# Kernel optimization log

Hardware: AMD Instinct MI355X
Metric: run time of the kernel (lower is better)

## Reference

```python
import jax, jax.numpy as jnp
import numpy as np
from jax import lax

DIM = 384
HEADS = 8

def setup_inputs() -> dict:
    key = jax.random.key(0)
    ks = jax.random.split(key, 7)
    B, C, H, W = 4, DIM, 128, 128
    x = jax.random.normal(ks[0], (B, C, H, W), dtype=jnp.float32)
    y = jax.random.normal(ks[1], (B, C, H, W), dtype=jnp.float32)
    s1 = 1.0 / np.sqrt(C)
    Wq = jax.random.normal(ks[2], (C, C), dtype=jnp.float32) * s1          # 1x1 conv [out,in]
    Wkv = jax.random.normal(ks[3], (2 * C, C), dtype=jnp.float32) * s1     # 1x1 conv
    Wdw = jax.random.normal(ks[4], (3 * C, 1, 3, 3), dtype=jnp.float32) * (1.0 / 3.0)  # depthwise 3x3
    Wproj = jax.random.normal(ks[5], (C, C), dtype=jnp.float32) * s1       # 1x1 conv
    temperature = jnp.ones((HEADS, 1, 1), dtype=jnp.float32)
    return {"x": x, "y": y, "Wq": Wq, "Wkv": Wkv, "Wdw": Wdw,
            "Wproj": Wproj, "temperature": temperature}


def _conv1x1(x, W):
    # x: [b,c,h,w], W: [o,c] -> [b,o,h,w]
    return jnp.einsum('bchw,oc->bohw', x, W)


def _l2norm(t, eps=1e-12):
    n = jnp.sqrt(jnp.sum(t * t, axis=-1, keepdims=True))
    return t / jnp.maximum(n, eps)


def reference(x, y, Wq, Wkv, Wdw, Wproj, temperature):
    b, c, h, w = x.shape
    q = _conv1x1(x, Wq)                     # [b,c,h,w]
    kv = _conv1x1(y, Wkv)                   # [b,2c,h,w]
    qkv = jnp.concatenate([q, kv], axis=1)  # [b,3c,h,w]
    qkv = lax.conv_general_dilated(
        qkv, Wdw, window_strides=(1, 1), padding='SAME',
        dimension_numbers=('NCHW', 'OIHW', 'NCHW'),
        feature_group_count=3 * c)
    q, k, v = jnp.split(qkv, 3, axis=1)
    cp = c // HEADS
    hw = h * w
    # b (head c) h w -> b head c (h w)
    q = q.reshape(b, HEADS, cp, hw)
    k = k.reshape(b, HEADS, cp, hw)
    v = v.reshape(b, HEADS, cp, hw)
    q = _l2norm(q)
    k = _l2norm(k)
    attn = jnp.einsum('bhcn,bhdn->bhcd', q, k) * temperature  # [b,head,cp,cp]
    attn = jax.nn.softmax(attn, axis=-1)
    out = jnp.einsum('bhcd,bhdn->bhcn', attn, v)              # [b,head,cp,hw]
    out = out.reshape(b, c, h, w)
    return _conv1x1(out, Wproj)
```

## Files before the change

### kernel.cpp

```cpp
#include <hip/hip_runtime.h>
#include <hip/hip_bf16.h>

#define DIM 384
#define HEADS 8
#define CP 48
#define NB 4
#define HIMG 128
#define WIMG 128
#define HW 16384

using bf16 = __hip_bfloat16;

typedef __attribute__((ext_vector_type(8))) short bf16x8;
typedef __attribute__((ext_vector_type(4))) float f32x4;

__device__ __forceinline__ float lo_bf(unsigned u){ union{unsigned i; float f;} c; c.i = u<<16; return c.f; }
__device__ __forceinline__ float hi_bf(unsigned u){ union{unsigned i; float f;} c; c.i = u & 0xffff0000u; return c.f; }
__device__ __forceinline__ bf16 f2bf(float v){ return __float2bfloat16(v); }
__device__ __forceinline__ unsigned short bfbits(float v){ union{ bf16 h; unsigned short u; } c; c.h = f2bf(v); return c.u; }

__device__ __forceinline__ float4 load4f(const float* p){ return *(const float4*)p; }
__device__ __forceinline__ float4 load4f(const bf16* p){
  uint2 u = *(const uint2*)p;
  float4 r; r.x = lo_bf(u.x); r.y = hi_bf(u.x); r.z = lo_bf(u.y); r.w = hi_bf(u.y); return r;
}

__device__ __forceinline__ void st(float* p, float v){ *p = v; }
__device__ __forceinline__ void st(bf16* p, float v){ *p = f2bf(v); }

#define GLD_LDS16(g, l) __builtin_amdgcn_global_load_lds( \
    (const __attribute__((address_space(1))) void*)(g), \
    (__attribute__((address_space(3))) void*)(l), 16, 0, 0)

__global__ __launch_bounds__(256) void convert_w(
    const float* __restrict__ Wq, const float* __restrict__ Wkv,
    bf16* __restrict__ Wq_bf, bf16* __restrict__ Wkv_bf)
{
  int idx = (blockIdx.x*256 + threadIdx.x) * 2;
  const int NQ = DIM*DIM;
  const int NKV = 2*DIM*DIM;
  if (idx < NQ) {
    unsigned u = (unsigned)bfbits(Wq[idx]) | ((unsigned)bfbits(Wq[idx+1]) << 16);
    *(unsigned*)(Wq_bf + idx) = u;
  } else {
    int j = idx - NQ;
    if (j < NKV) {
      unsigned u = (unsigned)bfbits(Wkv[j]) | ((unsigned)bfbits(Wkv[j+1]) << 16);
      *(unsigned*)(Wkv_bf + j) = u;
    }
  }
}

template<typename TIn>
__global__ __launch_bounds__(256) void transpose_cast(
    const TIn* __restrict__ in0, const TIn* __restrict__ in1,
    bf16* __restrict__ out0, bf16* __restrict__ out1,
    long inBatchStride, long outBatchStride)
{
  const int zb = blockIdx.z;
  const TIn* in = (zb < NB) ? in0 : in1;
  bf16* outp = (zb < NB) ? out0 : out1;
  const int b = zb & 3;
  const int n0 = blockIdx.x * 64;
  const int c0 = blockIdx.y * 64;
  const TIn* inb = in + (long)b * inBatchStride;
  bf16* outb = outp + (long)b * outBatchStride;

  __shared__ float tile[64][66];
  const int t = threadIdx.x;
#pragma unroll
  for (int i = 0; i < 4; ++i) {
    int g = i*256 + t;
    int r = g >> 4, c4 = g & 15;
    float4 v = load4f(inb + (long)(c0 + r)*HW + n0 + c4*4);
    tile[r][c4*4+0] = v.x; tile[r][c4*4+1] = v.y;
    tile[r][c4*4+2] = v.z; tile[r][c4*4+3] = v.w;
  }
  __syncthreads();
#pragma unroll
  for (int i = 0; i < 8; ++i) {
    int g = i*256 + t;
    int n = g >> 5, cu = g & 31;
    unsigned u = (unsigned)bfbits(tile[cu*2][n]) | ((unsigned)bfbits(tile[cu*2+1][n]) << 16);
    *(unsigned*)(outb + (long)(n0 + n)*DIM + c0 + cu*2) = u;
  }
}

template<typename TOut>
__global__ __launch_bounds__(256) void gemm_mfma(
    const bf16* __restrict__ A, long aStride,
    const bf16* __restrict__ Bt, TOut* __restrict__ C, int M, int K)
{
  const int b  = blockIdx.z;
  const int m0 = blockIdx.y * 128;
  const int n0 = blockIdx.x * 128;
  const bf16* Ab  = A  + (long)b * aStride;
  const bf16* Btb = Bt + (long)b * (long)HW * K;
  TOut* Cb = C + (long)b * (long)M * HW;

  __shared__ short As[128*64];
  __shared__ short Bs[128*64];

  const int t = threadIdx.x;
  const int w = t >> 6, lane = t & 63;
  const int quad = lane >> 4, l16 = lane & 15;
  const int wm = (w >> 1) * 64, wn = (w & 1) * 64;

  const bf16* gA[4]; const bf16* gB[4];
#pragma unroll
  for (int i = 0; i < 4; ++i) {
    int f = w*256 + i*64 + lane;
    int r = f >> 3, p = f & 7;
    int c = p ^ (r & 7);
    gA[i] = Ab  + (long)(m0 + r)*K + c*8;
    gB[i] = Btb + (long)(n0 + r)*K + c*8;
  }

  f32x4 acc[4][4] = {};

  for (int k0 = 0; k0 < K; k0 += 64) {
#pragma unroll
    for (int i = 0; i < 4; ++i) {
      GLD_LDS16(gA[i], As + (w*256 + i*64)*8);
      GLD_LDS16(gB[i], Bs + (w*256 + i*64)*8);
      gA[i] += 64; gB[i] += 64;
    }
    __syncthreads();
#pragma unroll
    for (int kk = 0; kk < 2; ++kk) {
      bf16x8 af[4], bfr[4];
      const int sw = (kk*4 + quad) ^ (l16 & 7);
#pragma unroll
      for (int mt = 0; mt < 4; ++mt) {
        af[mt]  = *(const bf16x8*)(As + (wm + mt*16 + l16)*64 + sw*8);
        bfr[mt] = *(const bf16x8*)(Bs + (wn + mt*16 + l16)*64 + sw*8);
      }
#pragma unroll
      for (int mt = 0; mt < 4; ++mt)
#pragma unroll
        for (int nt = 0; nt < 4; ++nt)
          acc[mt][nt] = __builtin_amdgcn_mfma_f32_16x16x32_bf16(af[mt], bfr[nt], acc[mt][nt], 0, 0, 0);
    }
    __syncthreads();
  }

#pragma unroll
  for (int mt = 0; mt < 4; ++mt)
#pragma unroll
    for (int nt = 0; nt < 4; ++nt)
#pragma unroll
      for (int j = 0; j < 4; ++j) {
        int row = m0 + wm + mt*16 + quad*4 + j;
        int col = n0 + wn + nt*16 + l16;
        st(Cb + (long)row*HW + col, acc[mt][nt][j]);
      }
}

__global__ __launch_bounds__(256) void dwconv_inplace(
    bf16* __restrict__ qb, bf16* __restrict__ kvb,
    const float* __restrict__ Wdw, float* __restrict__ ssq)
{
  const int ch = blockIdx.x;
  const int b  = blockIdx.y;
  bf16* plane = (ch < DIM) ? qb + ((long)b*DIM + ch)*HW
                           : kvb + ((long)b*2*DIM + (ch - DIM))*HW;
  float w9[9];
#pragma unroll
  for (int i = 0; i < 9; ++i) w9[i] = Wdw[ch*9 + i];

  __shared__ bf16 t_[128*140];
  const int t = threadIdx.x;
#pragma unroll
  for (int i = 0; i < 16; ++i) {
    int g = i*256 + t;
    int r = g >> 5, c4 = g & 31;
    *(uint2*)&t_[r*140 + c4*4] = *(const uint2*)(plane + r*128 + c4*4);
  }
  __syncthreads();

  const int r = t >> 1, half = t & 1, cbase = half*64;
  const float mtop = (r > 0)   ? 1.f : 0.f;
  const float mbot = (r < 127) ? 1.f : 0.f;
  const int rt = (r > 0)   ? r-1 : r;
  const int rb = (r < 127) ? r+1 : r;

  float a0,a1,a2,b0,b1,b2,c0,c1,c2;
#define LD3(cc, A, B, Cv) { A = __bfloat162float(t_[rt*140 + (cc)]) * mtop; \
                            B = __bfloat162float(t_[r*140 + (cc)]); \
                            Cv = __bfloat162float(t_[rb*140 + (cc)]) * mbot; }
  if (cbase == 0) { a0=b0=c0=0.f; } else LD3(cbase-1, a0, b0, c0);
  LD3(cbase,   a1, b1, c1);
  LD3(cbase+1, a2, b2, c2);

  float ss = 0.f;
  unsigned outu[32];
#pragma unroll 4
  for (int j = 0; j < 64; ++j) {
    float o = w9[0]*a0 + w9[1]*a1 + w9[2]*a2
            + w9[3]*b0 + w9[4]*b1 + w9[5]*b2
            + w9[6]*c0 + w9[7]*c1 + w9[8]*c2;
    ss += o*o;
    unsigned short ob = bfbits(o);
    if (j & 1) outu[j>>1] |= ((unsigned)ob << 16); else outu[j>>1] = ob;
    a0=a1; a1=a2; b0=b1; b1=b2; c0=c1; c1=c2;
    int nc = cbase + j + 2;
    if (nc <= 127) { LD3(nc, a2, b2, c2) } else { a2=b2=c2=0.f; }
  }
#undef LD3

#pragma unroll
  for (int i = 0; i < 8; ++i)
    *(uint4*)(plane + r*128 + cbase + i*8) = *(uint4*)&outu[i*4];

  if (ch < 2*DIM) {
#pragma unroll
    for (int off = 32; off; off >>= 1) ss += __shfl_down(ss, off);
    __shared__ float wsum[4];
    if ((t & 63) == 0) wsum[t >> 6] = ss;
    __syncthreads();
    if (t == 0) ssq[b*2*DIM + ch] = wsum[0]+wsum[1]+wsum[2]+wsum[3];
  }
}

__global__ __launch_bounds__(512) void s_mfma(
    const bf16* __restrict__ qd, const bf16* __restrict__ kd,
    float* __restrict__ Sp)
{
  const int split = blockIdx.x;
  const int h = blockIdx.y, b = blockIdx.z;
  const int t = threadIdx.x, w = t >> 6, lane = t & 63;
  const int quad = lane >> 4, l16 = lane & 15;
  const bf16* qp = qd + ((long)b*DIM + h*CP)*HW;
  const bf16* kp = kd + ((long)b*DIM + h*CP)*HW;
  const int nbase = (split*8 + w) * 256;

  f32x4 acc[3][3] = {};
  for (int ks = 0; ks < 8; ++ks) {
    const int n = nbase + ks*32 + quad*8;
    bf16x8 aq[3], bk[3];
#pragma unroll
    for (int i = 0; i < 3; ++i) {
      aq[i] = *(const bf16x8*)(qp + (long)(i*16 + l16)*HW + n);
      bk[i] = *(const bf16x8*)(kp + (long)(i*16 + l16)*HW + n);
    }
#pragma unroll
    for (int i = 0; i < 3; ++i)
#pragma unroll
      for (int j = 0; j < 3; ++j)
        acc[i][j] = __builtin_amdgcn_mfma_f32_16x16x32_bf16(aq[i], bk[j], acc[i][j], 0, 0, 0);
  }

  __shared__ float Sred[8][CP*CP];
#pragma unroll
  for (int i = 0; i < 3; ++i)
#pragma unroll
    for (int j = 0; j < 3; ++j)
#pragma unroll
      for (int rr = 0; rr < 4; ++rr)
        Sred[w][(i*16 + quad*4 + rr)*CP + j*16 + l16] = acc[i][j][rr];
  __syncthreads();

  float* out = Sp + (long)split*(NB*HEADS*CP*CP) + ((long)(b*HEADS + h))*CP*CP;
  for (int g = t; g < CP*CP; g += 512) {
    float s = 0.f;
#pragma unroll
    for (int ww = 0; ww < 8; ++ww) s += Sred[ww][g];
    out[g] = s;
  }
}

__global__ __launch_bounds__(64) void softmax_attn(
    float* __restrict__ Sp, const float* __restrict__ ssq,
    const float* __restrict__ temp)
{
  const int bhc = blockIdx.x;
  const int c = bhc % CP;
  const int h = (bhc / CP) % HEADS;
  const int b = bhc / (CP * HEADS);
  const int lane = threadIdx.x;
  const long rowoff = ((long)(b*HEADS + h))*CP*CP + c*CP;
  const float rq = rsqrtf(ssq[b*2*DIM + h*CP + c]);
  const float tmp = temp[h];
  float logit = -1e30f;
  if (lane < CP) {
    float s = 0.f;
#pragma unroll
    for (int sl = 0; sl < 8; ++sl) s += Sp[(long)sl*(NB*HEADS*CP*CP) + rowoff + lane];
    float rk = rsqrtf(ssq[b*2*DIM + DIM + h*CP + lane]);
    logit = s * rq * rk * tmp;
  }
  float m = logit;
#pragma unroll
  for (int off = 32; off; off >>= 1) m = fmaxf(m, __shfl_down(m, off));
  m = __shfl(m, 0);
  float e = (lane < CP) ? __expf(logit - m) : 0.f;
  float s = e;
#pragma unroll
  for (int off = 32; off; off >>= 1) s += __shfl_down(s, off);
  s = __shfl(s, 0);
  if (lane < CP) Sp[rowoff + lane] = e / s;
}

__global__ __launch_bounds__(256) void w2fold(
    const float* __restrict__ attn, const float* __restrict__ Wproj,
    bf16* __restrict__ W2)
{
  const int ot = blockIdx.x;
  const int h  = blockIdx.y;
  const int b  = blockIdx.z;
  __shared__ float at[CP][CP];
  __shared__ float wp[128][CP];
  const int t = threadIdx.x;
  const float* Ap = attn + ((long)(b*HEADS + h))*CP*CP;
#pragma unroll
  for (int i = 0; i < 9; ++i) {
    int idx = t + 256*i;
    at[idx / CP][idx % CP] = Ap[idx];
  }
#pragma unroll
  for (int i = 0; i < 24; ++i) {
    int idx = t + 256*i;
    int o = idx / CP, c = idx % CP;
    wp[o][c] = Wproj[(long)(ot*128 + o)*DIM + h*CP + c];
  }
  __syncthreads();
#pragma unroll
  for (int i = 0; i < 24; ++i) {
    int idx = t + 256*i;
    int o = idx / CP, d = idx % CP;
    float a = 0.f;
#pragma unroll
    for (int c = 0; c < CP; ++c) a += wp[o][c] * at[c][d];
    W2[((long)b*DIM + ot*128 + o)*DIM + h*CP + d] = f2bf(a);
  }
}

extern "C" void kernel_launch(void* const* d_in, const int* in_sizes, int n_in,
                              void* d_out, int out_size, void* d_ws, size_t ws_size,
                              hipStream_t stream) {
  const float* x     = (const float*)d_in[0];
  const float* y     = (const float*)d_in[1];
  const float* Wq    = (const float*)d_in[2];
  const float* Wkv   = (const float*)d_in[3];
  const float* Wdw   = (const float*)d_in[4];
  const float* Wproj = (const float*)d_in[5];
  const float* temp  = (const float*)d_in[6];
  float* out = (float*)d_out;

  char* ws = (char*)d_ws;
  const long SZ_T  = 50331648L;
  bf16* xT    = (bf16*)(ws + 0L);
  bf16* yT    = (bf16*)(ws + SZ_T);
  bf16* q_bf  = (bf16*)(ws + 2*SZ_T);
  bf16* kv_bf = (bf16*)(ws + 3*SZ_T);
  char* tail  = ws + 5*SZ_T;
  bf16* Wq_bf  = (bf16*)(tail);
  bf16* Wkv_bf = (bf16*)(tail + 294912L);
  float* Sp    = (float*)(tail);
  bf16* W2_bf  = (bf16*)(tail + 294912L);
  float* ssq   = (float*)(tail + 2359296L);
  bf16* vdT    = xT;
  bf16* vd     = kv_bf + (long)DIM*HW;

  convert_w<<<864, 256, 0, stream>>>(Wq, Wkv, Wq_bf, Wkv_bf);
  transpose_cast<float><<<dim3(HW/64, DIM/64, 8), 256, 0, stream>>>(
      x, y, xT, yT, (long)DIM*HW, (long)HW*DIM);
  gemm_mfma<bf16><<<dim3(HW/128, DIM/128, NB), 256, 0, stream>>>(
      Wq_bf, 0, xT, q_bf, DIM, DIM);
  gemm_mfma<bf16><<<dim3(HW/128, 2*DIM/128, NB), 256, 0, stream>>>(
      Wkv_bf, 0, yT, kv_bf, 2*DIM, DIM);
  dwconv_inplace<<<dim3(3*DIM, NB), 256, 0, stream>>>(q_bf, kv_bf, Wdw, ssq);
  transpose_cast<bf16><<<dim3(HW/64, DIM/64, NB), 256, 0, stream>>>(
      vd, nullptr, vdT, nullptr, (long)2*DIM*HW, (long)HW*DIM);
  s_mfma<<<dim3(8, HEADS, NB), 512, 0, stream>>>(q_bf, kv_bf, Sp);
  softmax_attn<<<dim3(NB*HEADS*CP), 64, 0, stream>>>(Sp, ssq, temp);
  w2fold<<<dim3(3, HEADS, NB), 256, 0, stream>>>(Sp, Wproj, W2_bf);
  gemm_mfma<float><<<dim3(HW/128, DIM/128, NB), 256, 0, stream>>>(
      W2_bf, (long)DIM*DIM, vdT, out, DIM, DIM);
}
```

Before: 560.7 us.

## Replace transpose+GEMM with panel GEMM that transposes B in LDS

```diff
diff --git a/kernel.cpp b/kernel.cpp
--- a/kernel.cpp
+++ b/kernel.cpp
@@ -17,20 +17,10 @@
 __device__ __forceinline__ float lo_bf(unsigned u){ union{unsigned i; float f;} c; c.i = u<<16; return c.f; }
 __device__ __forceinline__ float hi_bf(unsigned u){ union{unsigned i; float f;} c; c.i = u & 0xffff0000u; return c.f; }
 __device__ __forceinline__ bf16 f2bf(float v){ return __float2bfloat16(v); }
-__device__ __forceinline__ unsigned short bfbits(float v){ union{ bf16 h; unsigned short u; } c; c.h = f2bf(v); return c.u; }
-
-__device__ __forceinline__ float4 load4f(const float* p){ return *(const float4*)p; }
-__device__ __forceinline__ float4 load4f(const bf16* p){
-  uint2 u = *(const uint2*)p;
-  float4 r; r.x = lo_bf(u.x); r.y = hi_bf(u.x); r.z = lo_bf(u.y); r.w = hi_bf(u.y); return r;
-}
+__device__ __forceinline__ unsigned bfbits(float v){ union{ bf16 h; unsigned short u; } c; c.h = f2bf(v); return (unsigned)c.u; }
 
 __device__ __forceinline__ void st(float* p, float v){ *p = v; }
 __device__ __forceinline__ void st(bf16* p, float v){ *p = f2bf(v); }
-
-#define GLD_LDS16(g, l) __builtin_amdgcn_global_load_lds( \
-    (const __attribute__((address_space(1))) void*)(g), \
-    (__attribute__((address_space(3))) void*)(l), 16, 0, 0)
 
 __global__ __launch_bounds__(256) void convert_w(
     const float* __restrict__ Wq, const float* __restrict__ Wkv,
@@ -40,120 +30,103 @@
   const int NQ = DIM*DIM;
   const int NKV = 2*DIM*DIM;
   if (idx < NQ) {
-    unsigned u = (unsigned)bfbits(Wq[idx]) | ((unsigned)bfbits(Wq[idx+1]) << 16);
+    unsigned u = bfbits(Wq[idx]) | (bfbits(Wq[idx+1]) << 16);
     *(unsigned*)(Wq_bf + idx) = u;
   } else {
     int j = idx - NQ;
     if (j < NKV) {
-      unsigned u = (unsigned)bfbits(Wkv[j]) | ((unsigned)bfbits(Wkv[j+1]) << 16);
+      unsigned u = bfbits(Wkv[j]) | (bfbits(Wkv[j+1]) << 16);
       *(unsigned*)(Wkv_bf + j) = u;
     }
   }
 }
 
-template<typename TIn>
-__global__ __launch_bounds__(256) void transpose_cast(
-    const TIn* __restrict__ in0, const TIn* __restrict__ in1,
-    bf16* __restrict__ out0, bf16* __restrict__ out1,
-    long inBatchStride, long outBatchStride)
-{
-  const int zb = blockIdx.z;
-  const TIn* in = (zb < NB) ? in0 : in1;
-  bf16* outp = (zb < NB) ? out0 : out1;
-  const int b = zb & 3;
+template<typename TB, typename TOut>
+__global__ __launch_bounds__(256, 2) void gemm_bpanel(
+    const bf16* __restrict__ A, long aStride,
+    const TB* __restrict__ B, long bStride,
+    TOut* __restrict__ C, long cStride, int M)
+{
+  const int b  = blockIdx.z;
   const int n0 = blockIdx.x * 64;
-  const int c0 = blockIdx.y * 64;
-  const TIn* inb = in + (long)b * inBatchStride;
-  bf16* outb = outp + (long)b * outBatchStride;
-
-  __shared__ float tile[64][66];
-  const int t = threadIdx.x;
-#pragma unroll
-  for (int i = 0; i < 4; ++i) {
-    int g = i*256 + t;
-    int r = g >> 4, c4 = g & 15;
-    float4 v = load4f(inb + (long)(c0 + r)*HW + n0 + c4*4);
-    tile[r][c4*4+0] = v.x; tile[r][c4*4+1] = v.y;
-    tile[r][c4*4+2] = v.z; tile[r][c4*4+3] = v.w;
-  }
-  __syncthreads();
-#pragma unroll
-  for (int i = 0; i < 8; ++i) {
-    int g = i*256 + t;
-    int n = g >> 5, cu = g & 31;
-    unsigned u = (unsigned)bfbits(tile[cu*2][n]) | ((unsigned)bfbits(tile[cu*2+1][n]) << 16);
-    *(unsigned*)(outb + (long)(n0 + n)*DIM + c0 + cu*2) = u;
-  }
-}
-
-template<typename TOut>
-__global__ __launch_bounds__(256) void gemm_mfma(
-    const bf16* __restrict__ A, long aStride,
-    const bf16* __restrict__ Bt, TOut* __restrict__ C, int M, int K)
-{
-  const int b  = blockIdx.z;
-  const int m0 = blockIdx.y * 128;
-  const int n0 = blockIdx.x * 128;
-  const bf16* Ab  = A  + (long)b * aStride;
-  const bf16* Btb = Bt + (long)b * (long)HW * K;
-  TOut* Cb = C + (long)b * (long)M * HW;
-
-  __shared__ short As[128*64];
-  __shared__ short Bs[128*64];
+  const bf16* Ab = A + (long)b * aStride;
+  const TB*   Bb = B + (long)b * bStride;
+  TOut*       Cb = C + (long)b * cStride;
+
+  __shared__ short Bs[64*384];
+  __shared__ short R[128*64];
 
   const int t = threadIdx.x;
   const int w = t >> 6, lane = t & 63;
   const int quad = lane >> 4, l16 = lane & 15;
-  const int wm = (w >> 1) * 64, wn = (w & 1) * 64;
-
-  const bf16* gA[4]; const bf16* gB[4];
-#pragma unroll
-  for (int i = 0; i < 4; ++i) {
-    int f = w*256 + i*64 + lane;
-    int r = f >> 3, p = f & 7;
-    int c = p ^ (r & 7);
-    gA[i] = Ab  + (long)(m0 + r)*K + c*8;
-    gB[i] = Btb + (long)(n0 + r)*K + c*8;
-  }
-
-  f32x4 acc[4][4] = {};
-
-  for (int k0 = 0; k0 < K; k0 += 64) {
-#pragma unroll
-    for (int i = 0; i < 4; ++i) {
-      GLD_LDS16(gA[i], As + (w*256 + i*64)*8);
-      GLD_LDS16(gB[i], Bs + (w*256 + i*64)*8);
-      gA[i] += 64; gB[i] += 64;
+
+  for (int s = 0; s < 3; ++s) {
+    const int k0 = s * 128;
+    if constexpr (sizeof(TB) == 4) {
+#pragma unroll
+      for (int ii = 0; ii < 8; ++ii) {
+        int idx = ii*256 + t;
+        int kr = idx >> 4, c4 = idx & 15;
+        float4 v = *(const float4*)((const float*)Bb + (long)(k0+kr)*HW + n0 + c4*4);
+        unsigned u0 = bfbits(v.x) | (bfbits(v.y) << 16);
+        unsigned u1 = bfbits(v.z) | (bfbits(v.w) << 16);
+        uint2 pk; pk.x = u0; pk.y = u1;
+        *(uint2*)&R[kr*64 + c4*4] = pk;
+      }
+    } else {
+#pragma unroll
+      for (int ii = 0; ii < 4; ++ii) {
+        int idx = ii*256 + t;
+        int kr = idx >> 3, c8 = idx & 7;
+        *(uint4*)&R[kr*64 + c8*8] = *(const uint4*)((const bf16*)Bb + (long)(k0+kr)*HW + n0 + c8*8);
+      }
     }
     __syncthreads();
-#pragma unroll
-    for (int kk = 0; kk < 2; ++kk) {
-      bf16x8 af[4], bfr[4];
-      const int sw = (kk*4 + quad) ^ (l16 & 7);
-#pragma unroll
-      for (int mt = 0; mt < 4; ++mt) {
-        af[mt]  = *(const bf16x8*)(As + (wm + mt*16 + l16)*64 + sw*8);
-        bfr[mt] = *(const bf16x8*)(Bs + (wn + mt*16 + l16)*64 + sw*8);
+    const int n = t & 63, kc0 = t >> 6;
+#pragma unroll
+    for (int jj = 0; jj < 4; ++jj) {
+      int kc = kc0 + jj*4;
+      bf16x8 val;
+#pragma unroll
+      for (int u = 0; u < 8; ++u) val[u] = R[(kc*8 + u)*64 + n];
+      int g = (s*16 + kc) ^ (n & 7);
+      *(bf16x8*)&Bs[n*384 + g*8] = val;
+    }
+    __syncthreads();
+  }
+
+  for (int mb = 0; mb < M; mb += 384) {
+    const int mw = mb + w*96;
+    f32x4 acc[6][4] = {};
+    for (int ks = 0; ks < 12; ++ks) {
+      const int kq = ks*32 + quad*8;
+      bf16x8 af[6];
+#pragma unroll
+      for (int mt = 0; mt < 6; ++mt)
+        af[mt] = *(const bf16x8*)(Ab + (long)(mw + mt*16 + l16)*384 + kq);
+      bf16x8 bfr[4];
+#pragma unroll
+      for (int nt = 0; nt < 4; ++nt) {
+        int g = (ks*4 + quad) ^ (l16 & 7);
+        bfr[nt] = *(const bf16x8*)&Bs[(nt*16 + l16)*384 + g*8];
       }
 #pragma unroll
-      for (int mt = 0; mt < 4; ++mt)
+      for (int mt = 0; mt < 6; ++mt)
 #pragma unroll
         for (int nt = 0; nt < 4; ++nt)
           acc[mt][nt] = __builtin_amdgcn_mfma_f32_16x16x32_bf16(af[mt], bfr[nt], acc[mt][nt], 0, 0, 0);
     }
-    __syncthreads();
-  }
-
-#pragma unroll
-  for (int mt = 0; mt < 4; ++mt)
-#pragma unroll
-    for (int nt = 0; nt < 4; ++nt)
-#pragma unroll
-      for (int j = 0; j < 4; ++j) {
-        int row = m0 + wm + mt*16 + quad*4 + j;
-        int col = n0 + wn + nt*16 + l16;
-        st(Cb + (long)row*HW + col, acc[mt][nt][j]);
-      }
+#pragma unroll
+    for (int mt = 0; mt < 6; ++mt)
+#pragma unroll
+      for (int nt = 0; nt < 4; ++nt)
+#pragma unroll
+        for (int j = 0; j < 4; ++j) {
+          int row = mw + mt*16 + quad*4 + j;
+          int col = n0 + nt*16 + l16;
+          st(Cb + (long)row*HW + col, acc[mt][nt][j]);
+        }
+  }
 }
 
 __global__ __launch_bounds__(256) void dwconv_inplace(
@@ -168,7 +141,7 @@
 #pragma unroll
   for (int i = 0; i < 9; ++i) w9[i] = Wdw[ch*9 + i];
 
-  __shared__ bf16 t_[128*140];
+  __shared__ __align__(16) bf16 t_[128*140];
   const int t = threadIdx.x;
 #pragma unroll
   for (int i = 0; i < 16; ++i) {
@@ -200,17 +173,27 @@
             + w9[3]*b0 + w9[4]*b1 + w9[5]*b2
             + w9[6]*c0 + w9[7]*c1 + w9[8]*c2;
     ss += o*o;
-    unsigned short ob = bfbits(o);
-    if (j & 1) outu[j>>1] |= ((unsigned)ob << 16); else outu[j>>1] = ob;
+    unsigned ob = bfbits(o);
+    if (j & 1) outu[j>>1] |= (ob << 16); else outu[j>>1] = ob;
     a0=a1; a1=a2; b0=b1; b1=b2; c0=c1; c1=c2;
     int nc = cbase + j + 2;
     if (nc <= 127) { LD3(nc, a2, b2, c2) } else { a2=b2=c2=0.f; }
   }
 #undef LD3
 
-#pragma unroll
-  for (int i = 0; i < 8; ++i)
-    *(uint4*)(plane + r*128 + cbase + i*8) = *(uint4*)&outu[i*4];
+  __syncthreads();
+#pragma unroll
+  for (int j = 0; j < 8; ++j) {
+    int G = r*16 + half*8 + j;
+    *(uint4*)&t_[(G ^ (r & 7))*8] = *(uint4*)&outu[j*4];
+  }
+  __syncthreads();
+#pragma unroll
+  for (int i = 0; i < 8; ++i) {
+    int o = i*256 + t;
+    uint4 vv = *(uint4*)&t_[(o ^ ((o >> 4) & 7))*8];
+    *(uint4*)(plane + o*8) = vv;
+  }
 
   if (ch < 2*DIM) {
 #pragma unroll
@@ -231,7 +214,7 @@
   const int t = threadIdx.x, w = t >> 6, lane = t & 63;
   const int quad = lane >> 4, l16 = lane & 15;
   const bf16* qp = qd + ((long)b*DIM + h*CP)*HW;
-  const bf16* kp = kd + ((long)b*DIM + h*CP)*HW;
+  const bf16* kp = kd + ((long)b*2*DIM + h*CP)*HW;
   const int nbase = (split*8 + w) * 256;
 
   f32x4 acc[3][3] = {};
@@ -348,33 +331,25 @@
   float* out = (float*)d_out;
 
   char* ws = (char*)d_ws;
-  const long SZ_T  = 50331648L;
-  bf16* xT    = (bf16*)(ws + 0L);
-  bf16* yT    = (bf16*)(ws + SZ_T);
-  bf16* q_bf  = (bf16*)(ws + 2*SZ_T);
-  bf16* kv_bf = (bf16*)(ws + 3*SZ_T);
-  char* tail  = ws + 5*SZ_T;
+  bf16*  q_bf  = (bf16*)(ws + 0L);
+  bf16*  kv_bf = (bf16*)(ws + 50331648L);
+  char* tail   = ws + 150994944L;
   bf16* Wq_bf  = (bf16*)(tail);
   bf16* Wkv_bf = (bf16*)(tail + 294912L);
   float* Sp    = (float*)(tail);
   bf16* W2_bf  = (bf16*)(tail + 294912L);
   float* ssq   = (float*)(tail + 2359296L);
-  bf16* vdT    = xT;
   bf16* vd     = kv_bf + (long)DIM*HW;
 
   convert_w<<<864, 256, 0, stream>>>(Wq, Wkv, Wq_bf, Wkv_bf);
-  transpose_cast<float><<<dim3(HW/64, DIM/64, 8), 256, 0, stream>>>(
-      x, y, xT, yT, (long)DIM*HW, (long)HW*DIM);
-  gemm_mfma<bf16><<<dim3(HW/128, DIM/128, NB), 256, 0, stream>>>(
-      Wq_bf, 0, xT, q_bf, DIM, DIM);
-  gemm_mfma<bf16><<<dim3(HW/128, 2*DIM/128, NB), 256, 0, stream>>>(
-      Wkv_bf, 0, yT, kv_bf, 2*DIM, DIM);
+  gemm_bpanel<float, bf16><<<dim3(HW/64, 1, NB), 256, 0, stream>>>(
+      Wq_bf, 0, x, (long)DIM*HW, q_bf, (long)DIM*HW, DIM);
+  gemm_bpanel<float, bf16><<<dim3(HW/64, 1, NB), 256, 0, stream>>>(
+      Wkv_bf, 0, y, (long)DIM*HW, kv_bf, (long)2*DIM*HW, 2*DIM);
   dwconv_inplace<<<dim3(3*DIM, NB), 256, 0, stream>>>(q_bf, kv_bf, Wdw, ssq);
-  transpose_cast<bf16><<<dim3(HW/64, DIM/64, NB), 256, 0, stream>>>(
-      vd, nullptr, vdT, nullptr, (long)2*DIM*HW, (long)HW*DIM);
   s_mfma<<<dim3(8, HEADS, NB), 512, 0, stream>>>(q_bf, kv_bf, Sp);
   softmax_attn<<<dim3(NB*HEADS*CP), 64, 0, stream>>>(Sp, ssq, temp);
   w2fold<<<dim3(3, HEADS, NB), 256, 0, stream>>>(Sp, Wproj, W2_bf);
-  gemm_mfma<float><<<dim3(HW/128, DIM/128, NB), 256, 0, stream>>>(
-      W2_bf, (long)DIM*DIM, vdT, out, DIM, DIM);
-}
+  gemm_bpanel<bf16, float><<<dim3(HW/64, 1, NB), 256, 0, stream>>>(
+      W2_bf, (long)DIM*DIM, vd, (long)2*DIM*HW, out, (long)DIM*HW, DIM);
+}
```

After: 640.5 us. 1.14x slower.
